# Performance work log

Hardware: AMD Instinct MI355X
Metric: run time of the kernel (lower is better)

The kernel has to match this reference:

```python
import jax, jax.numpy as jnp
import numpy as np

SEQ, BATCH, IN, HID = 512, 64, 1024, 1024


def setup_inputs() -> dict:
    key = jax.random.key(0)
    ks = jax.random.split(key, 5)
    s = 1.0 / np.sqrt(HID)  # torch LSTM init scale
    return {
        "x": jax.random.normal(ks[0], (SEQ, BATCH, IN), dtype=jnp.float32),
        "W_ih": jax.random.uniform(ks[1], (4 * HID, IN), dtype=jnp.float32, minval=-s, maxval=s),
        "W_hh": jax.random.uniform(ks[2], (4 * HID, HID), dtype=jnp.float32, minval=-s, maxval=s),
        "b_ih": jax.random.uniform(ks[3], (4 * HID,), dtype=jnp.float32, minval=-s, maxval=s),
        "b_hh": jax.random.uniform(ks[4], (4 * HID,), dtype=jnp.float32, minval=-s, maxval=s),
    }


def reference(x, W_ih, W_hh, b_ih, b_hh):
    # Precompute input contribution to gates for all timesteps: [T, B, 4H]
    xg = jnp.einsum("tbi,gi->tbg", x, W_ih) + (b_ih + b_hh)
    W_hh_T = W_hh.T  # [H, 4H]

    def step(carry, xg_t):
        h, c = carry
        gates = xg_t + h @ W_hh_T  # [B, 4H]
        i, f, g, o = jnp.split(gates, 4, axis=-1)  # torch order: i, f, g, o
        c_new = jax.nn.sigmoid(f) * c + jax.nn.sigmoid(i) * jnp.tanh(g)
        h_new = jax.nn.sigmoid(o) * jnp.tanh(c_new)
        return (h_new, c_new), h_new

    B = x.shape[1]
    h0 = jnp.zeros((B, HID), dtype=x.dtype)
    c0 = jnp.zeros((B, HID), dtype=x.dtype)
    _, y = jax.lax.scan(step, (h0, c0), xg)
    return y  # [T, B, H]
```

## Files before the change

kernel.cpp:

```cpp
#include <hip/hip_runtime.h>

#define T_SEQ 512
#define BATCH 64
#define IN_F  1024
#define HID_F 1024
#define G4    4096

typedef __bf16 bf16x8 __attribute__((ext_vector_type(8)));
typedef float  f32x4  __attribute__((ext_vector_type(4)));
typedef unsigned short u16;
typedef unsigned int   u32;
typedef unsigned long long u64;

__device__ __forceinline__ u16 f2bf(float x) {
    u32 u = __builtin_bit_cast(u32, x);
    u = (u + 0x7FFFu + ((u >> 16) & 1u)) >> 16;
    return (u16)u;
}

__device__ __forceinline__ float sigf(float x) {
    return 1.0f / (1.0f + __expf(-x));
}
__device__ __forceinline__ float tanh_fast(float x) {
    float e = __expf(-2.0f * fabsf(x));
    float t = (1.0f - e) / (1.0f + e);
    return x < 0.0f ? -t : t;
}

__global__ void cast_bf16_k(const float* __restrict__ in, u16* __restrict__ out, long n4) {
    long i = (long)blockIdx.x * blockDim.x + threadIdx.x;
    long stride = (long)gridDim.x * blockDim.x;
    for (; i < n4; i += stride) {
        float4 v = ((const float4*)in)[i];
        ushort4 o = make_ushort4(f2bf(v.x), f2bf(v.y), f2bf(v.z), f2bf(v.w));
        ((ushort4*)out)[i] = o;
    }
}

__global__ __launch_bounds__(256) void xg_gemm_k(
    const u16* __restrict__ A, const u16* __restrict__ Bm,
    const float* __restrict__ bih, const float* __restrict__ bhh,
    float* __restrict__ out)
{
    __shared__ __align__(16) u16 As[128][40];
    __shared__ __align__(16) u16 Bs[128][40];

    const int tid  = threadIdx.x;
    const int bg   = blockIdx.y * 128;
    const int btb  = blockIdx.x * 128;
    const int lane = tid & 63;
    const int wid  = tid >> 6;
    const int wr   = wid >> 1;
    const int wc   = wid & 1;
    const int lrow = lane & 15;
    const int lq   = lane >> 4;

    f32x4 acc[4][4];
    #pragma unroll
    for (int i = 0; i < 4; ++i)
        #pragma unroll
        for (int j = 0; j < 4; ++j)
            acc[i][j] = (f32x4){0.f, 0.f, 0.f, 0.f};

    for (int k0 = 0; k0 < 1024; k0 += 32) {
        #pragma unroll
        for (int s = 0; s < 2; ++s) {
            int u   = tid + s * 256;
            int row = u >> 2;
            int ko  = (u & 3) * 8;
            *(uint4*)&As[row][ko] = *(const uint4*)&A [(size_t)(bg  + row) * 1024 + k0 + ko];
            *(uint4*)&Bs[row][ko] = *(const uint4*)&Bm[(size_t)(btb + row) * 1024 + k0 + ko];
        }
        __syncthreads();

        bf16x8 af[4], bf[4];
        #pragma unroll
        for (int i = 0; i < 4; ++i) {
            af[i] = *(const bf16x8*)&As[wr * 64 + i * 16 + lrow][lq * 8];
            bf[i] = *(const bf16x8*)&Bs[wc * 64 + i * 16 + lrow][lq * 8];
        }
        #pragma unroll
        for (int mi = 0; mi < 4; ++mi)
            #pragma unroll
            for (int ni = 0; ni < 4; ++ni)
                acc[mi][ni] = __builtin_amdgcn_mfma_f32_16x16x32_bf16(af[mi], bf[ni], acc[mi][ni], 0, 0, 0);
        __syncthreads();
    }

    float bsum[4][4];
    #pragma unroll
    for (int mi = 0; mi < 4; ++mi)
        #pragma unroll
        for (int r = 0; r < 4; ++r) {
            int g = bg + wr * 64 + mi * 16 + lq * 4 + r;
            bsum[mi][r] = bih[g] + bhh[g];
        }

    #pragma unroll
    for (int mi = 0; mi < 4; ++mi)
        #pragma unroll
        for (int ni = 0; ni < 4; ++ni)
            #pragma unroll
            for (int r = 0; r < 4; ++r) {
                int g  = bg + wr * 64 + mi * 16 + lq * 4 + r;
                int tb = btb + wc * 64 + ni * 16 + lrow;
                int t  = tb >> 6;
                int b  = tb & 63;
                out[((size_t)t * G4 + g) * 64 + b] = acc[mi][ni][r] + bsum[mi][r];
            }
}

__global__ __launch_bounds__(256, 1) void lstm_seq_k(
    const u16* __restrict__ Whh,
    u64* __restrict__ h0b,
    u64* __restrict__ h1b,
    float* __restrict__ cT,
    const float* __restrict__ xgT,
    float* __restrict__ y,
    unsigned* __restrict__ slots,
    int t0, int tc)
{
    __shared__ __align__(16) u16 hs[16 * 1024];
    __shared__ float Gs[16][17];

    const int tid  = threadIdx.x;
    const int lane = tid & 63;
    const int w    = tid >> 6;
    const int lq   = lane >> 4;
    const int lr   = lane & 15;
    const int bid  = blockIdx.x;
    const int jwg  = bid >> 2;
    const int quad = bid & 3;
    const int j0   = jwg * 16;
    const int b0   = quad * 16;
    unsigned* qslots = slots + quad * 64;

    const int gate = lr & 3;
    const int jja  = lr >> 2;
    const size_t woff = (size_t)(gate * 1024 + j0 + w * 4 + jja) * 1024 + lq * 8;
    bf16x8 af[32];
    #pragma unroll
    for (int kk = 0; kk < 32; ++kk)
        af[kk] = *(const bf16x8*)&Whh[woff + (size_t)kk * 32];

    const int jme = j0 + w * 4 + lq;
    const int bme = b0 + lr;
    float c = (t0 == 0) ? 0.0f : cT[(size_t)jme * 64 + bme];
    const int swl = lr & 7;

    for (int tt = 0; tt < tc; ++tt) {
        const int gstep = t0 + tt;
        const u64* __restrict__ hin = (gstep & 1) ? h1b : h0b;
        u64* __restrict__ hout      = (gstep & 1) ? h0b : h1b;
        const float* __restrict__ xg = xgT + (size_t)tt * (G4 * BATCH);

        float xgv[4];
        #pragma unroll
        for (int g = 0; g < 4; ++g)
            xgv[g] = xg[(size_t)(g * 1024 + jme) * 64 + bme];

        if (tt > 0) {
            const unsigned stamp = (unsigned)tt;
            if (w == 0) {
                while (true) {
                    unsigned v = __hip_atomic_load(&qslots[lane], __ATOMIC_RELAXED, __HIP_MEMORY_SCOPE_AGENT);
                    if (__all((int)(v >= stamp))) break;
                    __builtin_amdgcn_s_sleep(4);
                }
            }
            __syncthreads();
            asm volatile("" ::: "memory");
        }

        u64 hv[16];
        #pragma unroll
        for (int s = 0; s < 8; ++s) {
            int g = tid + s * 256;
            int row = g >> 7, col = g & 127;
            const u64* p = hin + (size_t)(b0 + row) * 256 + col * 2;
            hv[2 * s]     = __hip_atomic_load(p,     __ATOMIC_RELAXED, __HIP_MEMORY_SCOPE_AGENT);
            hv[2 * s + 1] = __hip_atomic_load(p + 1, __ATOMIC_RELAXED, __HIP_MEMORY_SCOPE_AGENT);
        }
        #pragma unroll
        for (int s = 0; s < 8; ++s) {
            int g = tid + s * 256;
            int row = g >> 7, col = g & 127;
            uint4 q;
            q.x = (u32)hv[2 * s];     q.y = (u32)(hv[2 * s] >> 32);
            q.z = (u32)hv[2 * s + 1]; q.w = (u32)(hv[2 * s + 1] >> 32);
            *(uint4*)&hs[row * 1024 + ((col ^ (row & 7)) * 8)] = q;
        }
        __syncthreads();

        f32x4 acc[4];
        #pragma unroll
        for (int q = 0; q < 4; ++q) acc[q] = (f32x4){0.f, 0.f, 0.f, 0.f};
        #pragma unroll
        for (int kk = 0; kk < 32; ++kk) {
            bf16x8 bf = *(const bf16x8*)&hs[lr * 1024 + (((lq + 4 * kk) ^ swl) * 8)];
            acc[kk & 3] = __builtin_amdgcn_mfma_f32_16x16x32_bf16(af[kk], bf, acc[kk & 3], 0, 0, 0);
        }
        f32x4 g4 = (acc[0] + acc[1]) + (acc[2] + acc[3]);

        float cn = sigf(g4[1] + xgv[1]) * c + sigf(g4[0] + xgv[0]) * tanh_fast(g4[2] + xgv[2]);
        float hn = sigf(g4[3] + xgv[3]) * tanh_fast(cn);
        c = cn;

        float h1 = __shfl(hn, lr + 16);
        float h2 = __shfl(hn, lr + 32);
        float h3 = __shfl(hn, lr + 48);
        if (lq == 0) {
            u64 pv = (u64)f2bf(hn) | ((u64)f2bf(h1) << 16) |
                     ((u64)f2bf(h2) << 32) | ((u64)f2bf(h3) << 48);
            __hip_atomic_store(hout + (size_t)(b0 + lr) * 256 + (j0 >> 2) + w, pv,
                               __ATOMIC_RELAXED, __HIP_MEMORY_SCOPE_AGENT);
        }
        Gs[w * 4 + lq][lr] = hn;

        asm volatile("s_waitcnt vmcnt(0)" ::: "memory");
        __syncthreads();
        if (tid == 0)
            __hip_atomic_store(&qslots[jwg], (unsigned)(tt + 1),
                               __ATOMIC_RELAXED, __HIP_MEMORY_SCOPE_AGENT);

        int bb = tid >> 4, jj = tid & 15;
        float* yt = y + (size_t)gstep * (BATCH * HID_F);
        yt[(size_t)(b0 + bb) * 1024 + j0 + jj] = Gs[jj][bb];
    }
    cT[(size_t)jme * 64 + bme] = c;
}

extern "C" void kernel_launch(void* const* d_in, const int* in_sizes, int n_in,
                              void* d_out, int out_size, void* d_ws, size_t ws_size,
                              hipStream_t stream) {
    const float* x    = (const float*)d_in[0];
    const float* Wih  = (const float*)d_in[1];
    const float* Whh  = (const float*)d_in[2];
    const float* bih  = (const float*)d_in[3];
    const float* bhh  = (const float*)d_in[4];
    float* y = (float*)d_out;

    char* ws = (char*)d_ws;
    size_t off = 0;
    auto alloc = [&](size_t bytes) { size_t p = off; off += (bytes + 255) & ~(size_t)255; return p; };

    unsigned* slots = (unsigned*)(ws + alloc(4 * 64 * 4));
    u16* xb    = (u16*)(ws + alloc((size_t)T_SEQ * BATCH * IN_F * 2));
    u16* wihb  = (u16*)(ws + alloc((size_t)G4 * IN_F * 2));
    u16* whhb  = (u16*)(ws + alloc((size_t)G4 * HID_F * 2));
    u64* hbuf0 = (u64*)(ws + alloc((size_t)BATCH * HID_F * 2));
    u64* hbuf1 = (u64*)(ws + alloc((size_t)BATCH * HID_F * 2));
    float* cT  = (float*)(ws + alloc((size_t)HID_F * BATCH * 4));

    size_t slot_bytes = (size_t)G4 * BATCH * 4;
    size_t remain = ws_size > off ? ws_size - off : 0;
    long ringT = (long)(remain / slot_bytes);
    if (ringT > T_SEQ) ringT = T_SEQ;
    ringT &= ~1L;
    if (ringT < 2) ringT = 2;
    float* xgT = (float*)(ws + alloc((size_t)ringT * slot_bytes));

    cast_bf16_k<<<2048, 256, 0, stream>>>(x,   xb,   (long)T_SEQ * BATCH * IN_F / 4);
    cast_bf16_k<<<512,  256, 0, stream>>>(Wih, wihb, (long)G4 * IN_F / 4);
    cast_bf16_k<<<512,  256, 0, stream>>>(Whh, whhb, (long)G4 * HID_F / 4);

    hipMemsetAsync(hbuf0, 0, (size_t)BATCH * HID_F * 2, stream);

    for (long t0 = 0; t0 < T_SEQ; t0 += ringT) {
        long tc = T_SEQ - t0 < ringT ? T_SEQ - t0 : ringT;
        dim3 ggrid((unsigned)(tc * BATCH / 128), G4 / 128);
        xg_gemm_k<<<ggrid, 256, 0, stream>>>(wihb, xb + (size_t)t0 * BATCH * IN_F, bih, bhh, xgT);
        hipMemsetAsync(slots, 0, 4 * 64 * 4, stream);
        lstm_seq_k<<<256, 256, 0, stream>>>(whhb, hbuf0, hbuf1, cT, xgT, y, slots, (int)t0, (int)tc);
    }
}
```

Before: 2.936 ms.

## Fuse input-gate GEMM into persistent LSTM kernel with producer-consumer overlap

Merges the separate input-projection GEMM and the sequential LSTM recurrence into one launch of 512 blocks. Blocks 256 and up compute xg tiles in time order and bump a per-timestep-pair done counter. The first 256 blocks spin on both the h-step slots and that counter before reading xg. This is meant to hide the GEMM behind the latency-bound recurrence and drop a launch. The risks are that all 512 blocks must be co-resident (launch bounds now allow 2 per CU), that the GEMM blocks compete with the recurrence for CU resources, and that xg stores now go through relaxed atomics.

```diff
diff --git a/kernel.cpp b/kernel.cpp
--- a/kernel.cpp
+++ b/kernel.cpp
@@ -37,97 +37,107 @@
     }
 }
 
-__global__ __launch_bounds__(256) void xg_gemm_k(
-    const u16* __restrict__ A, const u16* __restrict__ Bm,
-    const float* __restrict__ bih, const float* __restrict__ bhh,
-    float* __restrict__ out)
-{
-    __shared__ __align__(16) u16 As[128][40];
-    __shared__ __align__(16) u16 Bs[128][40];
-
-    const int tid  = threadIdx.x;
-    const int bg   = blockIdx.y * 128;
-    const int btb  = blockIdx.x * 128;
-    const int lane = tid & 63;
-    const int wid  = tid >> 6;
-    const int wr   = wid >> 1;
-    const int wc   = wid & 1;
-    const int lrow = lane & 15;
-    const int lq   = lane >> 4;
-
-    f32x4 acc[4][4];
-    #pragma unroll
-    for (int i = 0; i < 4; ++i)
-        #pragma unroll
-        for (int j = 0; j < 4; ++j)
-            acc[i][j] = (f32x4){0.f, 0.f, 0.f, 0.f};
-
-    for (int k0 = 0; k0 < 1024; k0 += 32) {
-        #pragma unroll
-        for (int s = 0; s < 2; ++s) {
-            int u   = tid + s * 256;
-            int row = u >> 2;
-            int ko  = (u & 3) * 8;
-            *(uint4*)&As[row][ko] = *(const uint4*)&A [(size_t)(bg  + row) * 1024 + k0 + ko];
-            *(uint4*)&Bs[row][ko] = *(const uint4*)&Bm[(size_t)(btb + row) * 1024 + k0 + ko];
-        }
-        __syncthreads();
-
-        bf16x8 af[4], bf[4];
-        #pragma unroll
-        for (int i = 0; i < 4; ++i) {
-            af[i] = *(const bf16x8*)&As[wr * 64 + i * 16 + lrow][lq * 8];
-            bf[i] = *(const bf16x8*)&Bs[wc * 64 + i * 16 + lrow][lq * 8];
-        }
-        #pragma unroll
-        for (int mi = 0; mi < 4; ++mi)
-            #pragma unroll
-            for (int ni = 0; ni < 4; ++ni)
-                acc[mi][ni] = __builtin_amdgcn_mfma_f32_16x16x32_bf16(af[mi], bf[ni], acc[mi][ni], 0, 0, 0);
-        __syncthreads();
-    }
-
-    float bsum[4][4];
-    #pragma unroll
-    for (int mi = 0; mi < 4; ++mi)
-        #pragma unroll
-        for (int r = 0; r < 4; ++r) {
-            int g = bg + wr * 64 + mi * 16 + lq * 4 + r;
-            bsum[mi][r] = bih[g] + bhh[g];
-        }
-
-    #pragma unroll
-    for (int mi = 0; mi < 4; ++mi)
-        #pragma unroll
-        for (int ni = 0; ni < 4; ++ni)
-            #pragma unroll
-            for (int r = 0; r < 4; ++r) {
-                int g  = bg + wr * 64 + mi * 16 + lq * 4 + r;
-                int tb = btb + wc * 64 + ni * 16 + lrow;
-                int t  = tb >> 6;
-                int b  = tb & 63;
-                out[((size_t)t * G4 + g) * 64 + b] = acc[mi][ni][r] + bsum[mi][r];
-            }
-}
-
-__global__ __launch_bounds__(256, 1) void lstm_seq_k(
+__global__ __launch_bounds__(256, 2) void fused_k(
     const u16* __restrict__ Whh,
+    const u16* __restrict__ Wih,
+    const u16* __restrict__ xb,
     u64* __restrict__ h0b,
     u64* __restrict__ h1b,
     float* __restrict__ cT,
-    const float* __restrict__ xgT,
+    float* __restrict__ xgT,
     float* __restrict__ y,
+    const float* __restrict__ bih, const float* __restrict__ bhh,
     unsigned* __restrict__ slots,
+    unsigned* __restrict__ done,
     int t0, int tc)
 {
     __shared__ __align__(16) u16 hs[16 * 1024];
     __shared__ float Gs[16][17];
+    __shared__ __align__(16) u16 As[128][40];
+    __shared__ __align__(16) u16 Bs[128][40];
 
     const int tid  = threadIdx.x;
     const int lane = tid & 63;
     const int w    = tid >> 6;
     const int lq   = lane >> 4;
     const int lr   = lane & 15;
+
+    if (blockIdx.x >= 256) {
+        const int p = blockIdx.x - 256;
+        const int ntb = (tc * BATCH) / 128;
+        const int ntiles = ntb * 32;
+        const u16* __restrict__ Bm = xb + (size_t)t0 * BATCH * IN_F;
+        const int wid  = tid >> 6;
+        const int wr   = wid >> 1;
+        const int wc   = wid & 1;
+
+        for (int i = p; i < ntiles; i += 256) {
+            const int tbt = i >> 5;
+            const int bg  = (i & 31) * 128;
+            const int btb = tbt * 128;
+
+            f32x4 acc[4][4];
+            #pragma unroll
+            for (int a = 0; a < 4; ++a)
+                #pragma unroll
+                for (int b = 0; b < 4; ++b)
+                    acc[a][b] = (f32x4){0.f, 0.f, 0.f, 0.f};
+
+            for (int k0 = 0; k0 < 1024; k0 += 32) {
+                #pragma unroll
+                for (int s = 0; s < 2; ++s) {
+                    int u   = tid + s * 256;
+                    int row = u >> 2;
+                    int ko  = (u & 3) * 8;
+                    *(uint4*)&As[row][ko] = *(const uint4*)&Wih[(size_t)(bg  + row) * 1024 + k0 + ko];
+                    *(uint4*)&Bs[row][ko] = *(const uint4*)&Bm [(size_t)(btb + row) * 1024 + k0 + ko];
+                }
+                __syncthreads();
+
+                bf16x8 af[4], bf[4];
+                #pragma unroll
+                for (int a = 0; a < 4; ++a) {
+                    af[a] = *(const bf16x8*)&As[wr * 64 + a * 16 + lr][lq * 8];
+                    bf[a] = *(const bf16x8*)&Bs[wc * 64 + a * 16 + lr][lq * 8];
+                }
+                #pragma unroll
+                for (int mi = 0; mi < 4; ++mi)
+                    #pragma unroll
+                    for (int ni = 0; ni < 4; ++ni)
+                        acc[mi][ni] = __builtin_amdgcn_mfma_f32_16x16x32_bf16(af[mi], bf[ni], acc[mi][ni], 0, 0, 0);
+                __syncthreads();
+            }
+
+            #pragma unroll
+            for (int mi = 0; mi < 4; ++mi) {
+                float bsum[4];
+                #pragma unroll
+                for (int r = 0; r < 4; ++r) {
+                    int g = bg + wr * 64 + mi * 16 + lq * 4 + r;
+                    bsum[r] = bih[g] + bhh[g];
+                }
+                #pragma unroll
+                for (int ni = 0; ni < 4; ++ni)
+                    #pragma unroll
+                    for (int r = 0; r < 4; ++r) {
+                        int g  = bg + wr * 64 + mi * 16 + lq * 4 + r;
+                        int tb = btb + wc * 64 + ni * 16 + lr;
+                        int t  = tb >> 6;
+                        int b  = tb & 63;
+                        __hip_atomic_store(&xgT[((size_t)t * G4 + g) * 64 + b],
+                                           acc[mi][ni][r] + bsum[r],
+                                           __ATOMIC_RELAXED, __HIP_MEMORY_SCOPE_AGENT);
+                    }
+            }
+
+            asm volatile("s_waitcnt vmcnt(0)" ::: "memory");
+            __syncthreads();
+            if (tid == 0)
+                __hip_atomic_fetch_add(&done[tbt], 1u, __ATOMIC_RELAXED, __HIP_MEMORY_SCOPE_AGENT);
+        }
+        return;
+    }
+
     const int bid  = blockIdx.x;
     const int jwg  = bid >> 2;
     const int quad = bid & 3;
@@ -153,24 +163,27 @@
         const u64* __restrict__ hin = (gstep & 1) ? h1b : h0b;
         u64* __restrict__ hout      = (gstep & 1) ? h0b : h1b;
         const float* __restrict__ xg = xgT + (size_t)tt * (G4 * BATCH);
-
-        float xgv[4];
-        #pragma unroll
-        for (int g = 0; g < 4; ++g)
-            xgv[g] = xg[(size_t)(g * 1024 + jme) * 64 + bme];
-
-        if (tt > 0) {
+        const int tbt = tt >> 1;
+
+        {
             const unsigned stamp = (unsigned)tt;
             if (w == 0) {
                 while (true) {
-                    unsigned v = __hip_atomic_load(&qslots[lane], __ATOMIC_RELAXED, __HIP_MEMORY_SCOPE_AGENT);
-                    if (__all((int)(v >= stamp))) break;
-                    __builtin_amdgcn_s_sleep(4);
+                    unsigned vs = __hip_atomic_load(&qslots[lane], __ATOMIC_RELAXED, __HIP_MEMORY_SCOPE_AGENT);
+                    unsigned vd = __hip_atomic_load(&done[tbt],   __ATOMIC_RELAXED, __HIP_MEMORY_SCOPE_AGENT);
+                    if (__all((int)(vs >= stamp && vd >= 32u))) break;
+                    __builtin_amdgcn_s_sleep(1);
                 }
             }
             __syncthreads();
             asm volatile("" ::: "memory");
         }
+
+        float xgv[4];
+        #pragma unroll
+        for (int g = 0; g < 4; ++g)
+            xgv[g] = __hip_atomic_load(&xg[(size_t)(g * 1024 + jme) * 64 + bme],
+                                       __ATOMIC_RELAXED, __HIP_MEMORY_SCOPE_AGENT);
 
         u64 hv[16];
         #pragma unroll
@@ -244,7 +257,8 @@
     size_t off = 0;
     auto alloc = [&](size_t bytes) { size_t p = off; off += (bytes + 255) & ~(size_t)255; return p; };
 
-    unsigned* slots = (unsigned*)(ws + alloc(4 * 64 * 4));
+    unsigned* slots = (unsigned*)(ws + alloc(4 * 64 * 4 + 256 * 4));
+    unsigned* done  = slots + 4 * 64;
     u16* xb    = (u16*)(ws + alloc((size_t)T_SEQ * BATCH * IN_F * 2));
     u16* wihb  = (u16*)(ws + alloc((size_t)G4 * IN_F * 2));
     u16* whhb  = (u16*)(ws + alloc((size_t)G4 * HID_F * 2));
@@ -268,9 +282,8 @@
 
     for (long t0 = 0; t0 < T_SEQ; t0 += ringT) {
         long tc = T_SEQ - t0 < ringT ? T_SEQ - t0 : ringT;
-        dim3 ggrid((unsigned)(tc * BATCH / 128), G4 / 128);
-        xg_gemm_k<<<ggrid, 256, 0, stream>>>(wihb, xb + (size_t)t0 * BATCH * IN_F, bih, bhh, xgT);
-        hipMemsetAsync(slots, 0, 4 * 64 * 4, stream);
-        lstm_seq_k<<<256, 256, 0, stream>>>(whhb, hbuf0, hbuf1, cT, xgT, y, slots, (int)t0, (int)tc);
-    }
-}
+        hipMemsetAsync(slots, 0, 4 * 64 * 4 + 256 * 4, stream);
+        fused_k<<<512, 256, 0, stream>>>(whhb, wihb, xb, hbuf0, hbuf1, cT, xgT, y,
+                                         bih, bhh, slots, done, (int)t0, (int)tc);
+    }
+}
```

Result: slower. 3.059 ms (+4.2%).

## Replace slot-counter barrier with per-cell stamped hidden-state words

Applied to the files above, without the earlier changes.

Removes the separate per-quad slot array and its flag wait. Each 64-bit hidden-state cell now carries two bf16 values plus a timestep stamp, and consumers spin on each cell's stamp directly. This drops the store-drain wait, the extra barrier and the flag round trip on the critical per-step path. In exchange the hidden buffer doubles in size, reads carry half payload per load, and many more polling loads may retry per step.

```diff
diff --git a/kernel.cpp b/kernel.cpp
--- a/kernel.cpp
+++ b/kernel.cpp
@@ -112,12 +112,11 @@
 
 __global__ __launch_bounds__(256, 1) void lstm_seq_k(
     const u16* __restrict__ Whh,
-    u64* __restrict__ h0b,
-    u64* __restrict__ h1b,
+    u64* __restrict__ h0c,
+    u64* __restrict__ h1c,
     float* __restrict__ cT,
     const float* __restrict__ xgT,
     float* __restrict__ y,
-    unsigned* __restrict__ slots,
     int t0, int tc)
 {
     __shared__ __align__(16) u16 hs[16 * 1024];
@@ -133,7 +132,6 @@
     const int quad = bid & 3;
     const int j0   = jwg * 16;
     const int b0   = quad * 16;
-    unsigned* qslots = slots + quad * 64;
 
     const int gate = lr & 3;
     const int jja  = lr >> 2;
@@ -147,48 +145,47 @@
     const int bme = b0 + lr;
     float c = (t0 == 0) ? 0.0f : cT[(size_t)jme * 64 + bme];
     const int swl = lr & 7;
+    const int cellme = (j0 + 4 * w + lq) >> 1;
 
     for (int tt = 0; tt < tc; ++tt) {
         const int gstep = t0 + tt;
-        const u64* __restrict__ hin = (gstep & 1) ? h1b : h0b;
-        u64* __restrict__ hout      = (gstep & 1) ? h0b : h1b;
+        const u64* __restrict__ hin = (gstep & 1) ? h1c : h0c;
+        u64* __restrict__ hout      = (gstep & 1) ? h0c : h1c;
         const float* __restrict__ xg = xgT + (size_t)tt * (G4 * BATCH);
+        const u32 stampexp = (u32)gstep;
 
         float xgv[4];
         #pragma unroll
         for (int g = 0; g < 4; ++g)
             xgv[g] = xg[(size_t)(g * 1024 + jme) * 64 + bme];
 
-        if (tt > 0) {
-            const unsigned stamp = (unsigned)tt;
-            if (w == 0) {
-                while (true) {
-                    unsigned v = __hip_atomic_load(&qslots[lane], __ATOMIC_RELAXED, __HIP_MEMORY_SCOPE_AGENT);
-                    if (__all((int)(v >= stamp))) break;
-                    __builtin_amdgcn_s_sleep(4);
+        u32 pv[32];
+        #pragma unroll
+        for (int ph = 0; ph < 2; ++ph) {
+            u64 v[16];
+            #pragma unroll
+            for (int s = 0; s < 16; ++s) {
+                int g = tid + (ph * 16 + s) * 256;
+                v[s] = __hip_atomic_load(&hin[(size_t)(b0 + (g >> 9)) * 512 + (g & 511)],
+                                         __ATOMIC_RELAXED, __HIP_MEMORY_SCOPE_AGENT);
+            }
+            #pragma unroll
+            for (int s = 0; s < 16; ++s) {
+                int g = tid + (ph * 16 + s) * 256;
+                const u64* p = &hin[(size_t)(b0 + (g >> 9)) * 512 + (g & 511)];
+                while ((u32)(v[s] >> 32) != stampexp) {
+                    __builtin_amdgcn_s_sleep(1);
+                    v[s] = __hip_atomic_load(p, __ATOMIC_RELAXED, __HIP_MEMORY_SCOPE_AGENT);
                 }
+                pv[ph * 16 + s] = (u32)v[s];
             }
-            __syncthreads();
-            asm volatile("" ::: "memory");
-        }
-
-        u64 hv[16];
-        #pragma unroll
-        for (int s = 0; s < 8; ++s) {
-            int g = tid + s * 256;
-            int row = g >> 7, col = g & 127;
-            const u64* p = hin + (size_t)(b0 + row) * 256 + col * 2;
-            hv[2 * s]     = __hip_atomic_load(p,     __ATOMIC_RELAXED, __HIP_MEMORY_SCOPE_AGENT);
-            hv[2 * s + 1] = __hip_atomic_load(p + 1, __ATOMIC_RELAXED, __HIP_MEMORY_SCOPE_AGENT);
-        }
-        #pragma unroll
-        for (int s = 0; s < 8; ++s) {
-            int g = tid + s * 256;
-            int row = g >> 7, col = g & 127;
-            uint4 q;
-            q.x = (u32)hv[2 * s];     q.y = (u32)(hv[2 * s] >> 32);
-            q.z = (u32)hv[2 * s + 1]; q.w = (u32)(hv[2 * s + 1] >> 32);
-            *(uint4*)&hs[row * 1024 + ((col ^ (row & 7)) * 8)] = q;
+        }
+        #pragma unroll
+        for (int s2 = 0; s2 < 32; ++s2) {
+            int g = tid + s2 * 256;
+            int row = g >> 9, p = g & 511;
+            int u = p >> 2;
+            *(u32*)((char*)hs + row * 2048 + ((u ^ (row & 7)) * 16) + (p & 3) * 4) = pv[s2];
         }
         __syncthreads();
 
@@ -206,23 +203,15 @@
         float hn = sigf(g4[3] + xgv[3]) * tanh_fast(cn);
         c = cn;
 
-        float h1 = __shfl(hn, lr + 16);
-        float h2 = __shfl(hn, lr + 32);
-        float h3 = __shfl(hn, lr + 48);
-        if (lq == 0) {
-            u64 pv = (u64)f2bf(hn) | ((u64)f2bf(h1) << 16) |
-                     ((u64)f2bf(h2) << 32) | ((u64)f2bf(h3) << 48);
-            __hip_atomic_store(hout + (size_t)(b0 + lr) * 256 + (j0 >> 2) + w, pv,
+        float hp = __shfl(hn, (lane + 16) & 63);
+        if ((lq & 1) == 0) {
+            u64 cell = (u64)f2bf(hn) | ((u64)f2bf(hp) << 16) | ((u64)(u32)(gstep + 1) << 32);
+            __hip_atomic_store(&hout[(size_t)(b0 + lr) * 512 + cellme], cell,
                                __ATOMIC_RELAXED, __HIP_MEMORY_SCOPE_AGENT);
         }
+
         Gs[w * 4 + lq][lr] = hn;
-
-        asm volatile("s_waitcnt vmcnt(0)" ::: "memory");
-        __syncthreads();
-        if (tid == 0)
-            __hip_atomic_store(&qslots[jwg], (unsigned)(tt + 1),
-                               __ATOMIC_RELAXED, __HIP_MEMORY_SCOPE_AGENT);
-
+        __syncthreads();
         int bb = tid >> 4, jj = tid & 15;
         float* yt = y + (size_t)gstep * (BATCH * HID_F);
         yt[(size_t)(b0 + bb) * 1024 + j0 + jj] = Gs[jj][bb];
@@ -244,12 +233,11 @@
     size_t off = 0;
     auto alloc = [&](size_t bytes) { size_t p = off; off += (bytes + 255) & ~(size_t)255; return p; };
 
-    unsigned* slots = (unsigned*)(ws + alloc(4 * 64 * 4));
     u16* xb    = (u16*)(ws + alloc((size_t)T_SEQ * BATCH * IN_F * 2));
     u16* wihb  = (u16*)(ws + alloc((size_t)G4 * IN_F * 2));
     u16* whhb  = (u16*)(ws + alloc((size_t)G4 * HID_F * 2));
-    u64* hbuf0 = (u64*)(ws + alloc((size_t)BATCH * HID_F * 2));
-    u64* hbuf1 = (u64*)(ws + alloc((size_t)BATCH * HID_F * 2));
+    u64* hbuf0 = (u64*)(ws + alloc((size_t)BATCH * 512 * 8));
+    u64* hbuf1 = (u64*)(ws + alloc((size_t)BATCH * 512 * 8));
     float* cT  = (float*)(ws + alloc((size_t)HID_F * BATCH * 4));
 
     size_t slot_bytes = (size_t)G4 * BATCH * 4;
@@ -264,13 +252,12 @@
     cast_bf16_k<<<512,  256, 0, stream>>>(Wih, wihb, (long)G4 * IN_F / 4);
     cast_bf16_k<<<512,  256, 0, stream>>>(Whh, whhb, (long)G4 * HID_F / 4);
 
-    hipMemsetAsync(hbuf0, 0, (size_t)BATCH * HID_F * 2, stream);
+    hipMemsetAsync(hbuf0, 0, (size_t)BATCH * 512 * 8 * 2, stream);
 
     for (long t0 = 0; t0 < T_SEQ; t0 += ringT) {
         long tc = T_SEQ - t0 < ringT ? T_SEQ - t0 : ringT;
         dim3 ggrid((unsigned)(tc * BATCH / 128), G4 / 128);
         xg_gemm_k<<<ggrid, 256, 0, stream>>>(wihb, xb + (size_t)t0 * BATCH * IN_F, bih, bhh, xgT);
-        hipMemsetAsync(slots, 0, 4 * 64 * 4, stream);
-        lstm_seq_k<<<256, 256, 0, stream>>>(whhb, hbuf0, hbuf1, cT, xgT, y, slots, (int)t0, (int)tc);
-    }
-}
+        lstm_seq_k<<<256, 256, 0, stream>>>(whhb, hbuf0, hbuf1, cT, xgT, y, (int)t0, (int)tc);
+    }
+}
```

After: 4.316 ms. 1.47x slower.

## Fuse input projection into persistent LSTM recurrence kernel, drop xg GEMM

Applied to the files above, without the earlier changes.

Removes the separate x·W_ih GEMM and its fp32 gate buffer. Each persistent block now keeps its slice of W_ih in 128KB of LDS and computes the input contribution inside the timestep loop, reading bf16 x directly. Bias is added in registers. This drops the large intermediate write and read and the host-side chunking, but it doubles the MFMA work on the serial critical path of every step and adds an extra barrier.

```diff
diff --git a/kernel.cpp b/kernel.cpp
--- a/kernel.cpp
+++ b/kernel.cpp
@@ -37,91 +37,19 @@
     }
 }
 
-__global__ __launch_bounds__(256) void xg_gemm_k(
-    const u16* __restrict__ A, const u16* __restrict__ Bm,
-    const float* __restrict__ bih, const float* __restrict__ bhh,
-    float* __restrict__ out)
-{
-    __shared__ __align__(16) u16 As[128][40];
-    __shared__ __align__(16) u16 Bs[128][40];
-
-    const int tid  = threadIdx.x;
-    const int bg   = blockIdx.y * 128;
-    const int btb  = blockIdx.x * 128;
-    const int lane = tid & 63;
-    const int wid  = tid >> 6;
-    const int wr   = wid >> 1;
-    const int wc   = wid & 1;
-    const int lrow = lane & 15;
-    const int lq   = lane >> 4;
-
-    f32x4 acc[4][4];
-    #pragma unroll
-    for (int i = 0; i < 4; ++i)
-        #pragma unroll
-        for (int j = 0; j < 4; ++j)
-            acc[i][j] = (f32x4){0.f, 0.f, 0.f, 0.f};
-
-    for (int k0 = 0; k0 < 1024; k0 += 32) {
-        #pragma unroll
-        for (int s = 0; s < 2; ++s) {
-            int u   = tid + s * 256;
-            int row = u >> 2;
-            int ko  = (u & 3) * 8;
-            *(uint4*)&As[row][ko] = *(const uint4*)&A [(size_t)(bg  + row) * 1024 + k0 + ko];
-            *(uint4*)&Bs[row][ko] = *(const uint4*)&Bm[(size_t)(btb + row) * 1024 + k0 + ko];
-        }
-        __syncthreads();
-
-        bf16x8 af[4], bf[4];
-        #pragma unroll
-        for (int i = 0; i < 4; ++i) {
-            af[i] = *(const bf16x8*)&As[wr * 64 + i * 16 + lrow][lq * 8];
-            bf[i] = *(const bf16x8*)&Bs[wc * 64 + i * 16 + lrow][lq * 8];
-        }
-        #pragma unroll
-        for (int mi = 0; mi < 4; ++mi)
-            #pragma unroll
-            for (int ni = 0; ni < 4; ++ni)
-                acc[mi][ni] = __builtin_amdgcn_mfma_f32_16x16x32_bf16(af[mi], bf[ni], acc[mi][ni], 0, 0, 0);
-        __syncthreads();
-    }
-
-    float bsum[4][4];
-    #pragma unroll
-    for (int mi = 0; mi < 4; ++mi)
-        #pragma unroll
-        for (int r = 0; r < 4; ++r) {
-            int g = bg + wr * 64 + mi * 16 + lq * 4 + r;
-            bsum[mi][r] = bih[g] + bhh[g];
-        }
-
-    #pragma unroll
-    for (int mi = 0; mi < 4; ++mi)
-        #pragma unroll
-        for (int ni = 0; ni < 4; ++ni)
-            #pragma unroll
-            for (int r = 0; r < 4; ++r) {
-                int g  = bg + wr * 64 + mi * 16 + lq * 4 + r;
-                int tb = btb + wc * 64 + ni * 16 + lrow;
-                int t  = tb >> 6;
-                int b  = tb & 63;
-                out[((size_t)t * G4 + g) * 64 + b] = acc[mi][ni][r] + bsum[mi][r];
-            }
-}
-
 __global__ __launch_bounds__(256, 1) void lstm_seq_k(
     const u16* __restrict__ Whh,
+    const u16* __restrict__ Wih,
+    const u16* __restrict__ xb,
     u64* __restrict__ h0b,
     u64* __restrict__ h1b,
-    float* __restrict__ cT,
-    const float* __restrict__ xgT,
+    const float* __restrict__ bih, const float* __restrict__ bhh,
     float* __restrict__ y,
-    unsigned* __restrict__ slots,
-    int t0, int tc)
+    unsigned* __restrict__ slots)
 {
+    __shared__ __align__(16) u16 ws[64 * 1024];
     __shared__ __align__(16) u16 hs[16 * 1024];
-    __shared__ float Gs[16][17];
+    float* Gsp = (float*)hs;
 
     const int tid  = threadIdx.x;
     const int lane = tid & 63;
@@ -143,21 +71,32 @@
     for (int kk = 0; kk < 32; ++kk)
         af[kk] = *(const bf16x8*)&Whh[woff + (size_t)kk * 32];
 
+    #pragma unroll
+    for (int s = 0; s < 32; ++s) {
+        int u   = tid + s * 256;
+        int row = u >> 7;
+        int cu  = u & 127;
+        int grow = (row & 3) * 1024 + j0 + (row >> 4) * 4 + ((row >> 2) & 3);
+        *(uint4*)&ws[row * 1024 + ((cu ^ (row & 7)) * 8)] =
+            *(const uint4*)&Wih[(size_t)grow * 1024 + cu * 8];
+    }
+
     const int jme = j0 + w * 4 + lq;
     const int bme = b0 + lr;
-    float c = (t0 == 0) ? 0.0f : cT[(size_t)jme * 64 + bme];
+    float c = 0.0f;
     const int swl = lr & 7;
-
-    for (int tt = 0; tt < tc; ++tt) {
-        const int gstep = t0 + tt;
-        const u64* __restrict__ hin = (gstep & 1) ? h1b : h0b;
-        u64* __restrict__ hout      = (gstep & 1) ? h0b : h1b;
-        const float* __restrict__ xg = xgT + (size_t)tt * (G4 * BATCH);
-
-        float xgv[4];
-        #pragma unroll
-        for (int g = 0; g < 4; ++g)
-            xgv[g] = xg[(size_t)(g * 1024 + jme) * 64 + bme];
+    const int wsrow = (w * 16 + lr) * 1024;
+
+    float bs[4];
+    #pragma unroll
+    for (int g = 0; g < 4; ++g)
+        bs[g] = bih[g * 1024 + jme] + bhh[g * 1024 + jme];
+
+    __syncthreads();
+
+    for (int tt = 0; tt < T_SEQ; ++tt) {
+        const u64* __restrict__ hin = (tt & 1) ? h1b : h0b;
+        u64* __restrict__ hout      = (tt & 1) ? h0b : h1b;
 
         if (tt > 0) {
             const unsigned stamp = (unsigned)tt;
@@ -192,18 +131,28 @@
         }
         __syncthreads();
 
+        const u16* __restrict__ xrow = xb + ((size_t)tt * BATCH + b0 + lr) * 1024 + lq * 8;
+        bf16x8 bx[8];
+        #pragma unroll
+        for (int p = 0; p < 8; ++p)
+            bx[p] = *(const bf16x8*)(xrow + p * 32);
+
         f32x4 acc[4];
         #pragma unroll
         for (int q = 0; q < 4; ++q) acc[q] = (f32x4){0.f, 0.f, 0.f, 0.f};
         #pragma unroll
         for (int kk = 0; kk < 32; ++kk) {
-            bf16x8 bf = *(const bf16x8*)&hs[lr * 1024 + (((lq + 4 * kk) ^ swl) * 8)];
-            acc[kk & 3] = __builtin_amdgcn_mfma_f32_16x16x32_bf16(af[kk], bf, acc[kk & 3], 0, 0, 0);
+            bf16x8 bh = *(const bf16x8*)&hs[lr * 1024 + (((lq + 4 * kk) ^ swl) * 8)];
+            bf16x8 ax = *(const bf16x8*)&ws[wsrow + (((lq + 4 * kk) ^ swl) * 8)];
+            acc[kk & 3] = __builtin_amdgcn_mfma_f32_16x16x32_bf16(af[kk], bh, acc[kk & 3], 0, 0, 0);
+            acc[kk & 3] = __builtin_amdgcn_mfma_f32_16x16x32_bf16(ax, bx[kk & 7], acc[kk & 3], 0, 0, 0);
+            if (kk < 24)
+                bx[kk & 7] = *(const bf16x8*)(xrow + (kk + 8) * 32);
         }
         f32x4 g4 = (acc[0] + acc[1]) + (acc[2] + acc[3]);
 
-        float cn = sigf(g4[1] + xgv[1]) * c + sigf(g4[0] + xgv[0]) * tanh_fast(g4[2] + xgv[2]);
-        float hn = sigf(g4[3] + xgv[3]) * tanh_fast(cn);
+        float cn = sigf(g4[1] + bs[1]) * c + sigf(g4[0] + bs[0]) * tanh_fast(g4[2] + bs[2]);
+        float hn = sigf(g4[3] + bs[3]) * tanh_fast(cn);
         c = cn;
 
         float h1 = __shfl(hn, lr + 16);
@@ -215,7 +164,9 @@
             __hip_atomic_store(hout + (size_t)(b0 + lr) * 256 + (j0 >> 2) + w, pv,
                                __ATOMIC_RELAXED, __HIP_MEMORY_SCOPE_AGENT);
         }
-        Gs[w * 4 + lq][lr] = hn;
+
+        __syncthreads();
+        Gsp[(w * 4 + lq) * 17 + lr] = hn;
 
         asm volatile("s_waitcnt vmcnt(0)" ::: "memory");
         __syncthreads();
@@ -224,10 +175,9 @@
                                __ATOMIC_RELAXED, __HIP_MEMORY_SCOPE_AGENT);
 
         int bb = tid >> 4, jj = tid & 15;
-        float* yt = y + (size_t)gstep * (BATCH * HID_F);
-        yt[(size_t)(b0 + bb) * 1024 + j0 + jj] = Gs[jj][bb];
+        float* yt = y + (size_t)tt * (BATCH * HID_F);
+        yt[(size_t)(b0 + bb) * 1024 + j0 + jj] = Gsp[jj * 17 + bb];
     }
-    cT[(size_t)jme * 64 + bme] = c;
 }
 
 extern "C" void kernel_launch(void* const* d_in, const int* in_sizes, int n_in,
@@ -248,29 +198,15 @@
     u16* xb    = (u16*)(ws + alloc((size_t)T_SEQ * BATCH * IN_F * 2));
     u16* wihb  = (u16*)(ws + alloc((size_t)G4 * IN_F * 2));
     u16* whhb  = (u16*)(ws + alloc((size_t)G4 * HID_F * 2));
-    u64* hbuf0 = (u64*)(ws + alloc((size_t)BATCH * HID_F * 2));
-    u64* hbuf1 = (u64*)(ws + alloc((size_t)BATCH * HID_F * 2));
-    float* cT  = (float*)(ws + alloc((size_t)HID_F * BATCH * 4));
-
-    size_t slot_bytes = (size_t)G4 * BATCH * 4;
-    size_t remain = ws_size > off ? ws_size - off : 0;
-    long ringT = (long)(remain / slot_bytes);
-    if (ringT > T_SEQ) ringT = T_SEQ;
-    ringT &= ~1L;
-    if (ringT < 2) ringT = 2;
-    float* xgT = (float*)(ws + alloc((size_t)ringT * slot_bytes));
+    u64* hbuf0 = (u64*)(ws + alloc((size_t)BATCH * 256 * 8));
+    u64* hbuf1 = (u64*)(ws + alloc((size_t)BATCH * 256 * 8));
 
     cast_bf16_k<<<2048, 256, 0, stream>>>(x,   xb,   (long)T_SEQ * BATCH * IN_F / 4);
     cast_bf16_k<<<512,  256, 0, stream>>>(Wih, wihb, (long)G4 * IN_F / 4);
     cast_bf16_k<<<512,  256, 0, stream>>>(Whh, whhb, (long)G4 * HID_F / 4);
 
-    hipMemsetAsync(hbuf0, 0, (size_t)BATCH * HID_F * 2, stream);
-
-    for (long t0 = 0; t0 < T_SEQ; t0 += ringT) {
-        long tc = T_SEQ - t0 < ringT ? T_SEQ - t0 : ringT;
-        dim3 ggrid((unsigned)(tc * BATCH / 128), G4 / 128);
-        xg_gemm_k<<<ggrid, 256, 0, stream>>>(wihb, xb + (size_t)t0 * BATCH * IN_F, bih, bhh, xgT);
-        hipMemsetAsync(slots, 0, 4 * 64 * 4, stream);
-        lstm_seq_k<<<256, 256, 0, stream>>>(whhb, hbuf0, hbuf1, cT, xgT, y, slots, (int)t0, (int)tc);
-    }
-}
+    hipMemsetAsync(slots, 0, 4 * 64 * 4, stream);
+    hipMemsetAsync(hbuf0, 0, (size_t)BATCH * 256 * 8, stream);
+
+    lstm_seq_k<<<256, 256, 0, stream>>>(whhb, wihb, xb, hbuf0, hbuf1, bih, bhh, y, slots);
+}
```

Result: slower. 4.229 ms (+44.1%).
